# Kernel optimization log

Hardware: AMD Instinct MI355X
Metric: run time of the kernel (lower is better)

Reference implementation:

```python
import jax, jax.numpy as jnp
import numpy as np

NUM_CLASSES = 97  # vocab size; SOS token id == NUM_CLASSES
D = 512   # in_planes (xDim)
S = 512   # sDim (GRU hidden)
A = 512   # attDim == emdDim
T = 25    # max_len_labels == encoder length L
B = 2048  # batch


def setup_inputs() -> dict:
    key = jax.random.key(0)
    ks = jax.random.split(key, 15)
    r = lambda k, shp: jax.random.normal(k, shp, jnp.float32) * 0.05
    return dict(
        x=jax.random.normal(ks[0], (B, T, D), jnp.float32),
        targets=jax.random.randint(ks[1], (2, B, T), 0, NUM_CLASSES),  # (fwd, reversed)
        Wx=r(ks[2], (2, D, A)), bx=r(ks[3], (2, A)),
        Ws=r(ks[4], (2, S, A)), bs=r(ks[5], (2, A)),
        wv=r(ks[6], (2, A)), wvb=r(ks[7], (2,)),
        emb=r(ks[8], (2, NUM_CLASSES + 1, A)),
        Wih=r(ks[9], (2, 3 * S, D + A)), bih=r(ks[10], (2, 3 * S)),
        Whh=r(ks[11], (2, 3 * S, S)), bhh=r(ks[12], (2, 3 * S)),
        Wfc=r(ks[13], (2, NUM_CLASSES, S)), bfc=r(ks[14], (2, NUM_CLASSES)),
    )


def _decode(x, targets, Wx, bx, Ws, bs, wv, wvb, emb, Wih, bih, Whh, bhh, Wfc, bfc):
    """One DecoderUnit unrolled over T steps (teacher forcing). x: [B,L,D]."""
    Bn = x.shape[0]
    # xEmbed is step-invariant -> hoist out of the recurrence
    xProj = jnp.einsum('bld,da->bla', x, Wx) + bx  # [B,L,A]
    y0 = jnp.full((Bn, 1), NUM_CLASSES, dtype=targets.dtype)  # SOS at step 0
    y_seq = jnp.concatenate([y0, targets[:, :-1]], axis=1)     # [B,T]

    def step(s, y_prev):
        # Bahdanau attention
        sProj = s @ Ws + bs                                  # [B,A]
        e = jnp.tanh(sProj[:, None, :] + xProj) @ wv + wvb   # [B,L]
        alpha = jax.nn.softmax(e, axis=1)
        ctx = jnp.einsum('bl,bld->bd', alpha, x)             # [B,D]
        # single-step GRU (PyTorch gate convention: r, z, n)
        gin = jnp.concatenate([emb[y_prev], ctx], axis=1)    # [B, A+D]
        gi = gin @ Wih.T + bih                               # [B,3S]
        gh = s @ Whh.T + bhh
        ir, iz, inn = jnp.split(gi, 3, axis=1)
        hr, hz, hn = jnp.split(gh, 3, axis=1)
        r = jax.nn.sigmoid(ir + hr)
        z = jax.nn.sigmoid(iz + hz)
        n = jnp.tanh(inn + r * hn)
        s_new = (1.0 - z) * n + z * s
        return s_new, s_new @ Wfc.T + bfc                    # logits [B,C]

    s0 = jnp.zeros((Bn, S), x.dtype)
    _, outs = jax.lax.scan(step, s0, jnp.swapaxes(y_seq, 0, 1))  # [T,B,C]
    return jnp.swapaxes(outs, 0, 1)  # [B,T,C]


def reference(x, targets, Wx, bx, Ws, bs, wv, wvb, emb, Wih, bih, Whh, bhh, Wfc, bfc):
    # vmap over the 2 decoders (forward / reverse); x shared
    f = jax.vmap(_decode, in_axes=(None, 0) + (0,) * 13)
    return f(x, targets, Wx, bx, Ws, bs, wv, wvb, emb, Wih, bih, Whh, bhh, Wfc, bfc)  # [2,B,T,C]
```

## Files before the change

### kernel.cpp

```cpp
#include <hip/hip_runtime.h>
#include <hip/hip_fp16.h>

#define B_ 2048
#define T_ 25
#define CL_ 97

typedef float f32x4 __attribute__((ext_vector_type(4)));
typedef float f32x2 __attribute__((ext_vector_type(2)));
typedef _Float16 f16x8 __attribute__((ext_vector_type(8)));
typedef _Float16 f16x2 __attribute__((ext_vector_type(2)));

#define DI static __device__ __forceinline__

DI float fast_tanh(float x) { return 1.0f - 2.0f / (__expf(2.0f * x) + 1.0f); }
DI float fast_sigm(float x) { return 1.0f / (1.0f + __expf(-x)); }

DI void gl16(const void* g, void* l) {
    __builtin_amdgcn_global_load_lds((const __attribute__((address_space(1))) void*)g,
                                     (__attribute__((address_space(3))) void*)l, 16, 0, 0);
}


__global__ void k_convx(const float* __restrict__ x, _Float16* __restrict__ xh, int n8) {
    int i = blockIdx.x * 256 + threadIdx.x;
    if (i >= n8) return;
    const f32x4 v0 = *(const f32x4*)(x + (long long)i * 8);
    const f32x4 v1 = *(const f32x4*)(x + (long long)i * 8 + 4);
    f16x8 o;
    o[0] = (_Float16)v0[0]; o[1] = (_Float16)v0[1]; o[2] = (_Float16)v0[2]; o[3] = (_Float16)v0[3];
    o[4] = (_Float16)v1[0]; o[5] = (_Float16)v1[1]; o[6] = (_Float16)v1[2]; o[7] = (_Float16)v1[3];
    *(f16x8*)(xh + (long long)i * 8) = o;
}

__global__ void k_pack_w1(const float* __restrict__ Ws, const float* __restrict__ Whh,
                          const float* __restrict__ Wfc, const float* __restrict__ bs,
                          const float* __restrict__ bhh, const float* __restrict__ bfc,
                          _Float16* __restrict__ w1, float* __restrict__ b1) {
    int idx = blockIdx.x * 256 + threadIdx.x;
    if (idx >= 2 * 2176 * 64) return;
    const int k8 = idx & 63;
    const int n  = (idx >> 6) % 2176;
    const int g  = (idx >> 6) / 2176;
    const int k0 = k8 * 8;
    f16x8 o;
    if (n < 512) {
        const float* p = Ws + (long long)g * 512 * 512 + (long long)k0 * 512 + n;
        #pragma unroll
        for (int i = 0; i < 8; ++i) o[i] = (_Float16)p[(long long)i * 512];
    } else if (n < 2048) {
        const float* p = Whh + (long long)g * 1536 * 512 + (long long)(n - 512) * 512 + k0;
        #pragma unroll
        for (int i = 0; i < 8; ++i) o[i] = (_Float16)p[i];
    } else if (n < 2048 + CL_) {
        const float* p = Wfc + (long long)g * CL_ * 512 + (long long)(n - 2048) * 512 + k0;
        #pragma unroll
        for (int i = 0; i < 8; ++i) o[i] = (_Float16)p[i];
    } else {
        #pragma unroll
        for (int i = 0; i < 8; ++i) o[i] = (_Float16)0.0f;
    }
    *(f16x8*)(w1 + ((long long)g * 2176 + n) * 512 + k0) = o;
    if (k8 == 0) {
        float bv = (n < 512) ? bs[g * 512 + n]
                 : (n < 2048) ? bhh[g * 1536 + (n - 512)]
                 : (n < 2048 + CL_) ? bfc[g * CL_ + (n - 2048)] : 0.0f;
        b1[g * 2176 + n] = bv;
    }
}

__global__ void k_pack_w2(const float* __restrict__ Wih, _Float16* __restrict__ w2,
                          _Float16* __restrict__ w2e) {
    int idx = blockIdx.x * 256 + threadIdx.x;
    if (idx >= 2 * 1536 * 64) return;
    const int k8 = idx & 63;
    const int n  = (idx >> 6) % 1536;
    const int g  = (idx >> 6) / 1536;
    const int k0 = k8 * 8;
    const float* p = Wih + (long long)g * 1536 * 1024 + (long long)n * 1024;
    f16x8 o, oe;
    #pragma unroll
    for (int i = 0; i < 8; ++i) { o[i] = (_Float16)p[512 + k0 + i]; oe[i] = (_Float16)p[k0 + i]; }
    *(f16x8*)(w2  + ((long long)g * 1536 + n) * 512 + k0) = o;
    *(f16x8*)(w2e + ((long long)g * 1536 + n) * 512 + k0) = oe;
}

__global__ void k_pack_wx(const float* __restrict__ Wx, _Float16* __restrict__ wx) {
    int idx = blockIdx.x * 256 + threadIdx.x;
    if (idx >= 2 * 512 * 64) return;
    const int k8 = idx & 63;
    const int n  = (idx >> 6) & 511;
    const int g  = (idx >> 6) >> 9;
    const int k0 = k8 * 8;
    const float* p = Wx + (long long)g * 512 * 512 + (long long)k0 * 512 + n;
    f16x8 o;
    #pragma unroll
    for (int i = 0; i < 8; ++i) o[i] = (_Float16)p[(long long)i * 512];
    *(f16x8*)(wx + ((long long)g * 512 + n) * 512 + k0) = o;
}

__global__ void k_pack_emb(const float* __restrict__ emb, _Float16* __restrict__ embh) {
    int i = blockIdx.x * 256 + threadIdx.x;
    if (i >= 2 * 128 * 64) return;
    const int k8 = i & 63;
    const int y  = (i >> 6) & 127;
    const int g  = i >> 13;
    f16x8 o;
    if (y < 98) {
        const float* p = emb + (long long)(g * 98 + y) * 512 + k8 * 8;
        #pragma unroll
        for (int j = 0; j < 8; ++j) o[j] = (_Float16)p[j];
    } else {
        #pragma unroll
        for (int j = 0; j < 8; ++j) o[j] = (_Float16)0.0f;
    }
    *(f16x8*)(embh + (long long)(g * 128 + y) * 512 + k8 * 8) = o;
}

__global__ __launch_bounds__(256) void gemm_bt(
    const _Float16* __restrict__ A, long long aG,
    const _Float16* __restrict__ B, long long bG,
    float* __restrict__ Cf, _Float16* __restrict__ Ch,
    long long cG, int ldc,
    const float* __restrict__ bias, int biasG,
    int nblk_off, int n_split,
    float* __restrict__ lout, int lcols, int lldc)
{
    __shared__ _Float16 As[2][128 * 64];
    __shared__ _Float16 Bs[2][128 * 64];
    const int g  = blockIdx.z;
    const int m0 = blockIdx.y * 128;
    const int n0 = (blockIdx.x + nblk_off) * 128;
    const _Float16* Ag = A + (long long)g * aG + (long long)m0 * 512;
    const _Float16* Bg = B + (long long)g * bG + (long long)n0 * 512;
    const int tid  = threadIdx.x;
    const int lane = tid & 63, w = tid >> 6;
    const int wr = w >> 1, wc = w & 1;
    const int lr = lane & 15, kg = lane >> 4;
    const int srow = lane >> 3;
    const int scol = (((lane & 7) ^ srow) * 8);

    f32x4 acc[4][4];
    #pragma unroll
    for (int m = 0; m < 4; ++m)
        #pragma unroll
        for (int n = 0; n < 4; ++n) acc[m][n] = (f32x4)0.0f;

    auto stage = [&](int buf, int kt) {
        const int k0 = kt * 64;
        #pragma unroll
        for (int cc = 0; cc < 4; ++cc) {
            const int r = w * 32 + cc * 8;
            gl16(Ag + (long long)(r + srow) * 512 + k0 + scol, &As[buf][r * 64]);
            gl16(Bg + (long long)(r + srow) * 512 + k0 + scol, &Bs[buf][r * 64]);
        }
    };

    stage(0, 0);
    #pragma unroll
    for (int kt = 0; kt < 8; ++kt) {
        const int cur = kt & 1;
        if (kt < 7) {
            stage(cur ^ 1, kt + 1);
            asm volatile("s_waitcnt vmcnt(8)" ::: "memory");
        } else {
            asm volatile("s_waitcnt vmcnt(0)" ::: "memory");
        }
        __builtin_amdgcn_s_barrier();
        #pragma unroll
        for (int kk = 0; kk < 2; ++kk) {
            f16x8 af[4], bf[4];
            #pragma unroll
            for (int m = 0; m < 4; ++m) {
                const int R = wr * 64 + m * 16 + lr;
                af[m] = *(const f16x8*)&As[cur][R * 64 + (((kk * 4 + kg) ^ (R & 7)) * 8)];
            }
            #pragma unroll
            for (int n = 0; n < 4; ++n) {
                const int R = wc * 64 + n * 16 + lr;
                bf[n] = *(const f16x8*)&Bs[cur][R * 64 + (((kk * 4 + kg) ^ (R & 7)) * 8)];
            }
            #pragma unroll
            for (int m = 0; m < 4; ++m)
                #pragma unroll
                for (int n = 0; n < 4; ++n)
                    acc[m][n] = __builtin_amdgcn_mfma_f32_16x16x32_f16(af[m], bf[n], acc[m][n], 0, 0, 0);
        }
        __builtin_amdgcn_s_barrier();
    }

    #pragma unroll
    for (int n = 0; n < 4; ++n) {
        const int col = n0 + wc * 64 + n * 16 + lr;
        const float bb = bias ? bias[g * biasG + col] : 0.0f;
        if (col < n_split) {
            #pragma unroll
            for (int m = 0; m < 4; ++m) {
                const int row = m0 + wr * 64 + m * 16 + kg * 4;
                #pragma unroll
                for (int i = 0; i < 4; ++i) {
                    const long long off = (long long)g * cG + (long long)(row + i) * ldc + col;
                    const float v = acc[m][n][i] + bb;
                    if (Ch) Ch[off] = (_Float16)v; else Cf[off] = v;
                }
            }
        } else if (lout != nullptr) {
            const int c = col - n_split;
            if (c < lcols) {
                #pragma unroll
                for (int m = 0; m < 4; ++m) {
                    const int row = m0 + wr * 64 + m * 16 + kg * 4;
                    #pragma unroll
                    for (int i = 0; i < 4; ++i)
                        lout[(long long)(g * B_ + row + i) * lldc + c] = acc[m][n][i] + bb;
                }
            }
        }
    }
}

__global__ __launch_bounds__(256) void k_att(
    const _Float16* __restrict__ Yh,
    const _Float16* __restrict__ xpj,
    const _Float16* __restrict__ xh,
    const float* __restrict__ wv,
    _Float16* __restrict__ ctxh)
{
    const int b = blockIdx.x;
    const int tid = threadIdx.x, lane = tid & 63, w = tid >> 6;
    __shared__ float eL[2][28];
    __shared__ float red[2][4][512];
    const int a0 = lane * 8;

    #pragma unroll
    for (int g = 0; g < 2; ++g) {
        const _Float16* sp = Yh + (long long)(g * B_ + b) * 2048;
        const f16x8 spv = *(const f16x8*)(sp + a0);
        const float* wvg = wv + g * 512;
        const f32x4 wv0 = *(const f32x4*)(wvg + a0);
        const f32x4 wv1 = *(const f32x4*)(wvg + a0 + 4);
        const _Float16* xpb = xpj + (long long)(g * B_ + b) * 25 * 512;
        for (int l = w; l < 25; l += 4) {
            const f16x8 xv = *(const f16x8*)(xpb + l * 512 + a0);
            float part = 0.0f;
            #pragma unroll
            for (int i = 0; i < 4; ++i) {
                part += fast_tanh((float)spv[i]     + (float)xv[i])     * wv0[i];
                part += fast_tanh((float)spv[4 + i] + (float)xv[4 + i]) * wv1[i];
            }
            #pragma unroll
            for (int off = 32; off > 0; off >>= 1) part += __shfl_xor(part, off);
            if (lane == 0) eL[g][l] = part;
        }
    }
    __syncthreads();

    float al0[25], al1[25];
    float m0 = -1e30f, m1 = -1e30f;
    #pragma unroll
    for (int l = 0; l < 25; ++l) { m0 = fmaxf(m0, eL[0][l]); m1 = fmaxf(m1, eL[1][l]); }
    float ss0 = 0.0f, ss1 = 0.0f;
    #pragma unroll
    for (int l = 0; l < 25; ++l) {
        al0[l] = __expf(eL[0][l] - m0); ss0 += al0[l];
        al1[l] = __expf(eL[1][l] - m1); ss1 += al1[l];
    }
    const float inv0 = 1.0f / ss0, inv1 = 1.0f / ss1;

    float c0[8], c1[8];
    #pragma unroll
    for (int j = 0; j < 8; ++j) { c0[j] = 0.0f; c1[j] = 0.0f; }
    const _Float16* xb = xh + (long long)b * 25 * 512;
    #pragma unroll
    for (int l = 0; l < 25; ++l) {
        if ((l & 3) == w) {
            const f16x8 xv = *(const f16x8*)(xb + l * 512 + a0);
            #pragma unroll
            for (int j = 0; j < 8; ++j) {
                const float xf = (float)xv[j];
                c0[j] += al0[l] * xf;
                c1[j] += al1[l] * xf;
            }
        }
    }
    f32x4 p;
    #pragma unroll
    for (int h = 0; h < 2; ++h) {
        #pragma unroll
        for (int i = 0; i < 4; ++i) p[i] = c0[h * 4 + i] * inv0;
        *(f32x4*)&red[0][w][a0 + h * 4] = p;
        #pragma unroll
        for (int i = 0; i < 4; ++i) p[i] = c1[h * 4 + i] * inv1;
        *(f32x4*)&red[1][w][a0 + h * 4] = p;
    }
    __syncthreads();

    const int c = tid * 2;
    f32x2 s0 = {0.0f, 0.0f}, s1 = {0.0f, 0.0f};
    #pragma unroll
    for (int ww = 0; ww < 4; ++ww) {
        s0 += *(const f32x2*)&red[0][ww][c];
        s1 += *(const f32x2*)&red[1][ww][c];
    }
    f16x2 o0, o1;
    o0[0] = (_Float16)s0[0]; o0[1] = (_Float16)s0[1];
    o1[0] = (_Float16)s1[0]; o1[1] = (_Float16)s1[1];
    *(f16x2*)(ctxh + (long long)b * 512 + c) = o0;
    *(f16x2*)(ctxh + (long long)(B_ + b) * 512 + c) = o1;
}

__global__ void k_gate(const _Float16* __restrict__ Yh,
                       const _Float16* __restrict__ Y2h,
                       const float* __restrict__ eW,
                       const int* __restrict__ tgt,
                       float* __restrict__ s32, _Float16* __restrict__ sh, int t)
{
    const int idx = blockIdx.x * 256 + threadIdx.x;
    if (idx >= 2 * B_ * 256) return;
    const int jp = (idx & 255) * 2;
    const int b  = (idx >> 8) & (B_ - 1);
    const int g  = idx >> 19;
    const int y  = (t == 0) ? CL_ : tgt[(g * B_ + b) * T_ + t - 1];
    const float*    ew = eW  + (long long)(g * 128 + y) * 1536;
    const _Float16* y2 = Y2h + (long long)(g * B_ + b) * 1536;
    const _Float16* yy = Yh  + (long long)(g * B_ + b) * 2048;
    const f32x2 ewr = *(const f32x2*)(ew + jp);
    const f32x2 ewz = *(const f32x2*)(ew + 512 + jp);
    const f32x2 ewn = *(const f32x2*)(ew + 1024 + jp);
    const f16x2 y2r = *(const f16x2*)(y2 + jp);
    const f16x2 y2z = *(const f16x2*)(y2 + 512 + jp);
    const f16x2 y2n = *(const f16x2*)(y2 + 1024 + jp);
    const f16x2 ghr = *(const f16x2*)(yy + 512 + jp);
    const f16x2 ghz = *(const f16x2*)(yy + 1024 + jp);
    const f16x2 ghn = *(const f16x2*)(yy + 1536 + jp);
    const long long si = (long long)(g * B_ + b) * 512 + jp;
    const f32x2 so = *(const f32x2*)(s32 + si);
    f32x2 sn;
    f16x2 snh;
    #pragma unroll
    for (int i = 0; i < 2; ++i) {
        const float r  = fast_sigm(ewr[i] + (float)y2r[i] + (float)ghr[i]);
        const float z  = fast_sigm(ewz[i] + (float)y2z[i] + (float)ghz[i]);
        const float nn = fast_tanh(ewn[i] + (float)y2n[i] + r * (float)ghn[i]);
        sn[i]  = (1.0f - z) * nn + z * so[i];
        snh[i] = (_Float16)sn[i];
    }
    *(f32x2*)(s32 + si) = sn;
    *(f16x2*)(sh + si) = snh;
}

extern "C" void kernel_launch(void* const* d_in, const int* in_sizes, int n_in,
                              void* d_out, int out_size, void* d_ws, size_t ws_size,
                              hipStream_t stream)
{
    (void)in_sizes; (void)n_in; (void)out_size;
    const float* x   = (const float*)d_in[0];
    const int*   tgt = (const int*)d_in[1];
    const float* Wx  = (const float*)d_in[2];
    const float* bx  = (const float*)d_in[3];
    const float* Wsm = (const float*)d_in[4];
    const float* bs  = (const float*)d_in[5];
    const float* wv  = (const float*)d_in[6];
    const float* emb = (const float*)d_in[8];
    const float* Wih = (const float*)d_in[9];
    const float* bih = (const float*)d_in[10];
    const float* Whh = (const float*)d_in[11];
    const float* bhh = (const float*)d_in[12];
    const float* Wfc = (const float*)d_in[13];
    const float* bfc = (const float*)d_in[14];
    float* out = (float*)d_out;

    char* base = (char*)d_ws;
    size_t off = 0;
    auto alloc = [&](size_t bytes) -> void* {
        void* r = base + off;
        off = (off + bytes + 255) & ~(size_t)255;
        return r;
    };
    _Float16* xh   = (_Float16*)alloc((size_t)B_ * T_ * 512 * 2);
    _Float16* xpj  = (_Float16*)alloc((size_t)2 * B_ * T_ * 512 * 2);
    _Float16* w1   = (_Float16*)alloc((size_t)2 * 2176 * 512 * 2);
    _Float16* w2   = (_Float16*)alloc((size_t)2 * 1536 * 512 * 2);
    _Float16* w2e  = (_Float16*)alloc((size_t)2 * 1536 * 512 * 2);
    _Float16* wx   = (_Float16*)alloc((size_t)2 * 512 * 512 * 2);
    _Float16* embh = (_Float16*)alloc((size_t)2 * 128 * 512 * 2);
    float*    b1   = (float*)alloc((size_t)2 * 2176 * 4);
    float*    eW   = (float*)alloc((size_t)2 * 128 * 1536 * 4);
    float*    s32  = (float*)alloc((size_t)2 * B_ * 512 * 4);
    _Float16* sh   = (_Float16*)alloc((size_t)2 * B_ * 512 * 2);
    _Float16* ctx  = (_Float16*)alloc((size_t)2 * B_ * 512 * 2);
    _Float16* Yh   = (_Float16*)alloc((size_t)2 * B_ * 2048 * 2);
    _Float16* Y2h  = (_Float16*)alloc((size_t)2 * B_ * 1536 * 2);
    if (off > ws_size) return;

    hipMemsetAsync(s32, 0, (size_t)2 * B_ * 512 * 4, stream);
    hipMemsetAsync(sh,  0, (size_t)2 * B_ * 512 * 2, stream);

    k_convx   <<<12800, 256, 0, stream>>>(x, xh, (B_ * T_ * 512) / 8);
    k_pack_w1 <<<1088, 256, 0, stream>>>(Wsm, Whh, Wfc, bs, bhh, bfc, w1, b1);
    k_pack_w2 <<<768, 256, 0, stream>>>(Wih, w2, w2e);
    k_pack_wx <<<256, 256, 0, stream>>>(Wx, wx);
    k_pack_emb<<<64, 256, 0, stream>>>(emb, embh);

    gemm_bt<<<dim3(12, 1, 2), 256, 0, stream>>>(
        embh, 128ll * 512, w2e, 1536ll * 512, eW, nullptr,
        128ll * 1536, 1536, bih, 1536, 0, 1 << 30, nullptr, 0, 0);

    gemm_bt<<<dim3(4, 400, 2), 256, 0, stream>>>(
        xh, 0ll, wx, 512ll * 512, nullptr, xpj, (long long)B_ * T_ * 512, 512,
        bx, 512, 0, 1 << 30, nullptr, 0, 0);

    for (int t = 0; t < T_; ++t) {
        gemm_bt<<<dim3(t > 0 ? 17 : 16, 16, 2), 256, 0, stream>>>(
            sh, (long long)B_ * 512, w1, 2176ll * 512, nullptr, Yh,
            (long long)B_ * 2048, 2048, b1, 2176, 0, 2048,
            t > 0 ? out + (long long)(t - 1) * CL_ : nullptr, CL_, T_ * CL_);
        k_att<<<dim3(B_, 1, 1), 256, 0, stream>>>(Yh, xpj, xh, wv, ctx);
        gemm_bt<<<dim3(12, 16, 2), 256, 0, stream>>>(
            ctx, (long long)B_ * 512, w2, 1536ll * 512, nullptr, Y2h,
            (long long)B_ * 1536, 1536, nullptr, 0, 0, 1 << 30, nullptr, 0, 0);
        k_gate<<<4096, 256, 0, stream>>>(Yh, Y2h, eW, tgt, s32, sh, t);
    }
    gemm_bt<<<dim3(1, 16, 2), 256, 0, stream>>>(
        sh, (long long)B_ * 512, w1, 2176ll * 512, nullptr, Yh,
        (long long)B_ * 2048, 2048, b1, 2176, 16, 2048,
        out + 24ll * CL_, CL_, T_ * CL_);
}
```

Measured before the change: 2.987 ms.

## Single-buffer GEMM LDS and remap workgroups across XCDs for L2 locality

```diff
diff --git a/kernel.cpp b/kernel.cpp
--- a/kernel.cpp
+++ b/kernel.cpp
@@ -125,11 +125,18 @@
     int nblk_off, int n_split,
     float* __restrict__ lout, int lcols, int lldc)
 {
-    __shared__ _Float16 As[2][128 * 64];
-    __shared__ _Float16 Bs[2][128 * 64];
+    __shared__ _Float16 As[128 * 64];
+    __shared__ _Float16 Bs[128 * 64];
+    const int gx = gridDim.x, nwg = gx * gridDim.y;
+    const int o = blockIdx.y * gx + blockIdx.x;
+    const int q = nwg >> 3, r = nwg & 7;
+    const int xcd = o & 7, ii = o >> 3;
+    const int nn = (xcd < r ? xcd * (q + 1) : r * (q + 1) + (xcd - r) * q) + ii;
+    const int bx = nn % gx, by = nn / gx;
+
     const int g  = blockIdx.z;
-    const int m0 = blockIdx.y * 128;
-    const int n0 = (blockIdx.x + nblk_off) * 128;
+    const int m0 = by * 128;
+    const int n0 = (bx + nblk_off) * 128;
     const _Float16* Ag = A + (long long)g * aG + (long long)m0 * 512;
     const _Float16* Bg = B + (long long)g * bG + (long long)n0 * 512;
     const int tid  = threadIdx.x;
@@ -145,39 +152,29 @@
         #pragma unroll
         for (int n = 0; n < 4; ++n) acc[m][n] = (f32x4)0.0f;
 
-    auto stage = [&](int buf, int kt) {
+    #pragma unroll
+    for (int kt = 0; kt < 8; ++kt) {
         const int k0 = kt * 64;
+        __syncthreads();
         #pragma unroll
         for (int cc = 0; cc < 4; ++cc) {
-            const int r = w * 32 + cc * 8;
-            gl16(Ag + (long long)(r + srow) * 512 + k0 + scol, &As[buf][r * 64]);
-            gl16(Bg + (long long)(r + srow) * 512 + k0 + scol, &Bs[buf][r * 64]);
+            const int rr = w * 32 + cc * 8;
+            gl16(Ag + (long long)(rr + srow) * 512 + k0 + scol, &As[rr * 64]);
+            gl16(Bg + (long long)(rr + srow) * 512 + k0 + scol, &Bs[rr * 64]);
         }
-    };
-
-    stage(0, 0);
-    #pragma unroll
-    for (int kt = 0; kt < 8; ++kt) {
-        const int cur = kt & 1;
-        if (kt < 7) {
-            stage(cur ^ 1, kt + 1);
-            asm volatile("s_waitcnt vmcnt(8)" ::: "memory");
-        } else {
-            asm volatile("s_waitcnt vmcnt(0)" ::: "memory");
-        }
-        __builtin_amdgcn_s_barrier();
+        __syncthreads();
         #pragma unroll
         for (int kk = 0; kk < 2; ++kk) {
             f16x8 af[4], bf[4];
             #pragma unroll
             for (int m = 0; m < 4; ++m) {
                 const int R = wr * 64 + m * 16 + lr;
-                af[m] = *(const f16x8*)&As[cur][R * 64 + (((kk * 4 + kg) ^ (R & 7)) * 8)];
+                af[m] = *(const f16x8*)&As[R * 64 + (((kk * 4 + kg) ^ (R & 7)) * 8)];
             }
             #pragma unroll
             for (int n = 0; n < 4; ++n) {
                 const int R = wc * 64 + n * 16 + lr;
-                bf[n] = *(const f16x8*)&Bs[cur][R * 64 + (((kk * 4 + kg) ^ (R & 7)) * 8)];
+                bf[n] = *(const f16x8*)&Bs[R * 64 + (((kk * 4 + kg) ^ (R & 7)) * 8)];
             }
             #pragma unroll
             for (int m = 0; m < 4; ++m)
@@ -185,7 +182,6 @@
                 for (int n = 0; n < 4; ++n)
                     acc[m][n] = __builtin_amdgcn_mfma_f32_16x16x32_f16(af[m], bf[n], acc[m][n], 0, 0, 0);
         }
-        __builtin_amdgcn_s_barrier();
     }
 
     #pragma unroll
```

Result: faster. 2.675 ms (-10.4%).
